# Kernel tuning notes

Hardware: AMD Instinct MI355X
Metric: run time of the kernel (lower is better)

Reference implementation:

```python
import jax, jax.numpy as jnp
import numpy as np

EPS = 1e-12  # F.normalize denominator clamp


def setup_inputs() -> dict:
    key = jax.random.key(0)
    k1, k2, k3, k4 = jax.random.split(key, 4)
    bs, d, nc, ncl, cs, ny = 8192, 768, 64, 500, 100, 1000
    train_embedding = jax.random.normal(k1, (bs, d), dtype=jnp.float32)
    clusters = jax.random.normal(k2, (ncl, cs, d), dtype=jnp.float32)
    # init_concept: uniform in [-0.5, 0.5]
    concept = jax.random.uniform(k3, (d, nc), dtype=jnp.float32, minval=-0.5, maxval=0.5)
    W_h = jax.random.normal(k4, (d, ny), dtype=jnp.float32) * 0.02
    b_h = jnp.zeros((ny,), dtype=jnp.float32)
    return {"train_embedding": train_embedding, "clusters": clusters,
            "concept": concept, "W_h": W_h, "b_h": b_h}


def reference(train_embedding, clusters, concept, W_h, b_h):
    # column-wise L2 normalize concept (F.normalize p=2 dim=0)
    concept_normalized = concept / jnp.maximum(
        jnp.linalg.norm(concept, axis=0, keepdims=True), EPS)
    # projection onto span(concept): C (C^T C)^-1 C^T
    gram = concept.T @ concept                      # [nc, nc]
    proj_matrix = concept @ jnp.linalg.inv(gram) @ concept.T  # [d, d]
    proj = proj_matrix @ train_embedding.T          # [d, bs]
    cluster_mean = jnp.mean(clusters, axis=1)       # [ncl, d]
    score_matrix = jnp.abs(cluster_mean @ concept_normalized)  # [ncl, nc]
    score_norm = score_matrix / jnp.maximum(
        jnp.linalg.norm(score_matrix, axis=0, keepdims=True), EPS)
    L_sparse_1 = jnp.sum(score_norm)
    # sum_{i != j} <score_norm[:,i], score_norm[:,j]> == sum(G) - trace(G)
    G = score_norm.T @ score_norm                   # [nc, nc]
    L_sparse_2 = jnp.sum(G) - jnp.trace(G)
    y_pred = proj.T @ W_h + b_h                     # h_x as linear head, [bs, ny]
    return (y_pred, L_sparse_1, L_sparse_2)
```

## Files before the change

kernel.cpp:

```cpp
#include <hip/hip_runtime.h>
#include <hip/hip_bf16.h>
#include <math.h>

#define BS   8192
#define DD   768
#define NC   64
#define NCL  500
#define CS   100
#define NY   1000
#define EPSN 1e-12f

typedef __attribute__((ext_vector_type(8))) short bf16x8;
typedef __attribute__((ext_vector_type(4))) float f32x4;

union B8 { unsigned u[4]; bf16x8 v; uint4 q; };

__device__ inline unsigned short f2bf(float x) {
    __hip_bfloat16 h = __float2bfloat16(x);
    return *reinterpret_cast<unsigned short*>(&h);
}
__device__ inline unsigned pk2(float a, float b) {
    return (unsigned)f2bf(a) | ((unsigned)f2bf(b) << 16);
}

#define FMA4(acc, s, v) { (acc).x = fmaf((s), (v).x, (acc).x); \
                          (acc).y = fmaf((s), (v).y, (acc).y); \
                          (acc).z = fmaf((s), (v).z, (acc).z); \
                          (acc).w = fmaf((s), (v).w, (acc).w); }

__global__ __launch_bounds__(256) void k_front(
    const float* __restrict__ clusters, const float* __restrict__ C,
    const float* __restrict__ W, const float* __restrict__ X,
    float* __restrict__ gramP, float* __restrict__ Up,
    float* __restrict__ SP, unsigned short* __restrict__ Tb) {
    __shared__ __align__(16) char smem_raw[25600];
    int b = blockIdx.x, tid = threadIdx.x;
    if (b < 200) {
        int rt = b / 25, sp = b % 25;
        uint4 (*CbL)[64] = (uint4(*)[64])smem_raw;
        int r0 = rt * 64;
        int w  = tid >> 6, l = tid & 63;
        int rowA = r0 + w*16 + (l & 15);
        int rcl  = rowA < NCL ? rowA : (NCL - 1);
        int kq   = l >> 4;
        const float* ab = clusters + (size_t)rcl * CS * DD + (size_t)sp * 4 * DD + kq * 8;
        f32x4 acc[4];
        #pragma unroll
        for (int ng = 0; ng < 4; ++ng) acc[ng] = (f32x4){0.f, 0.f, 0.f, 0.f};
        for (int kc = 0; kc < DD; kc += 64) {
            __syncthreads();
            #pragma unroll
            for (int u = 0; u < 2; ++u) {
                int g = (tid >> 6) + u*4;
                int n = tid & 63;
                const float* cp = C + (size_t)(kc + g*8) * 64 + n;
                uint4 gr;
                gr.x = pk2(cp[0],   cp[64]);
                gr.y = pk2(cp[128], cp[192]);
                gr.z = pk2(cp[256], cp[320]);
                gr.w = pk2(cp[384], cp[448]);
                CbL[g][n] = gr;
            }
            __syncthreads();
            #pragma unroll
            for (int ss = 0; ss < 4; ++ss) {
                #pragma unroll
                for (int ks2 = 0; ks2 < 2; ++ks2) {
                    const float* ap = ab + (size_t)ss * DD + kc + ks2*32;
                    float4 xa = *((const float4*)ap);
                    float4 xc = *((const float4*)(ap + 4));
                    B8 a;
                    a.u[0] = pk2(xa.x, xa.y); a.u[1] = pk2(xa.z, xa.w);
                    a.u[2] = pk2(xc.x, xc.y); a.u[3] = pk2(xc.z, xc.w);
                    B8 b0, b1, b2, b3;
                    b0.q = CbL[ks2*4 + kq][(l & 15)];
                    b1.q = CbL[ks2*4 + kq][(l & 15) + 16];
                    b2.q = CbL[ks2*4 + kq][(l & 15) + 32];
                    b3.q = CbL[ks2*4 + kq][(l & 15) + 48];
                    acc[0] = __builtin_amdgcn_mfma_f32_16x16x32_bf16(a.v, b0.v, acc[0], 0, 0, 0);
                    acc[1] = __builtin_amdgcn_mfma_f32_16x16x32_bf16(a.v, b1.v, acc[1], 0, 0, 0);
                    acc[2] = __builtin_amdgcn_mfma_f32_16x16x32_bf16(a.v, b2.v, acc[2], 0, 0, 0);
                    acc[3] = __builtin_amdgcn_mfma_f32_16x16x32_bf16(a.v, b3.v, acc[3], 0, 0, 0);
                }
            }
        }
        int rw = r0 + w*16 + kq * 4;
        float* SPs = SP + (size_t)sp * 32768;
        #pragma unroll
        for (int ng = 0; ng < 4; ++ng) {
            int n = ng*16 + (l & 15);
            #pragma unroll
            for (int r = 0; r < 4; ++r)
                SPs[(size_t)(rw + r) * 64 + n] = acc[ng][r];
        }
    } else if (b < 328) {
        uint4 (*CbL)[64] = (uint4(*)[64])smem_raw;
        int r0 = (b - 200) * 64;
        int w  = tid >> 6, l = tid & 63;
        int rowA = r0 + w*16 + (l & 15);
        int kq   = l >> 4;
        const float* xb = X + (size_t)rowA * DD + kq * 8;
        f32x4 acc[4];
        #pragma unroll
        for (int ng = 0; ng < 4; ++ng) acc[ng] = (f32x4){0.f, 0.f, 0.f, 0.f};
        for (int kc = 0; kc < DD; kc += 64) {
            __syncthreads();
            #pragma unroll
            for (int u = 0; u < 2; ++u) {
                int g = (tid >> 6) + u*4;
                int n = tid & 63;
                const float* cp = C + (size_t)(kc + g*8) * 64 + n;
                uint4 gr;
                gr.x = pk2(cp[0],   cp[64]);
                gr.y = pk2(cp[128], cp[192]);
                gr.z = pk2(cp[256], cp[320]);
                gr.w = pk2(cp[384], cp[448]);
                CbL[g][n] = gr;
            }
            __syncthreads();
            #pragma unroll
            for (int ks2 = 0; ks2 < 2; ++ks2) {
                float4 xa = *((const float4*)(xb + kc + ks2*32));
                float4 xc = *((const float4*)(xb + kc + ks2*32 + 4));
                B8 a;
                a.u[0] = pk2(xa.x, xa.y); a.u[1] = pk2(xa.z, xa.w);
                a.u[2] = pk2(xc.x, xc.y); a.u[3] = pk2(xc.z, xc.w);
                B8 b0, b1, b2, b3;
                b0.q = CbL[ks2*4 + kq][(l & 15)];
                b1.q = CbL[ks2*4 + kq][(l & 15) + 16];
                b2.q = CbL[ks2*4 + kq][(l & 15) + 32];
                b3.q = CbL[ks2*4 + kq][(l & 15) + 48];
                acc[0] = __builtin_amdgcn_mfma_f32_16x16x32_bf16(a.v, b0.v, acc[0], 0, 0, 0);
                acc[1] = __builtin_amdgcn_mfma_f32_16x16x32_bf16(a.v, b1.v, acc[1], 0, 0, 0);
                acc[2] = __builtin_amdgcn_mfma_f32_16x16x32_bf16(a.v, b2.v, acc[2], 0, 0, 0);
                acc[3] = __builtin_amdgcn_mfma_f32_16x16x32_bf16(a.v, b3.v, acc[3], 0, 0, 0);
            }
        }
        int rw = r0 + w*16 + kq * 4;
        #pragma unroll
        for (int ng = 0; ng < 4; ++ng) {
            int n = ng*16 + (l & 15);
            #pragma unroll
            for (int r = 0; r < 4; ++r)
                Tb[(size_t)(rw + r) * 64 + n] = f2bf(acc[ng][r]);
        }
    } else if (b < 584) {
        int q  = b - 328;
        int j  = q & 63, ks = q >> 6;
        int i   = tid & 63;
        int seg = tid >> 6;
        int k0  = ks * 192 + seg * 48;
        float p = 0.f;
        for (int k = k0; k < k0 + 48; ++k)
            p += C[k * NC + i] * C[k * NC + j];
        float (*red)[64] = (float(*)[64])smem_raw;
        red[seg][i] = p;
        __syncthreads();
        if (seg == 0)
            gramP[(size_t)ks * 4096 + i * NC + j] =
                red[0][i] + red[1][i] + red[2][i] + red[3][i];
    } else {
        int q  = b - 584;
        int nt = q >> 2, ks = q & 3;
        int n0 = nt * 128, kb = ks * 192;
        float (*Cu)[68]  = (float(*)[68])smem_raw;
        float (*Wu)[132] = (float(*)[132])(smem_raw + 8704);
        int tx = tid & 15, ty = tid >> 4;
        float4 a0[4], a1[4];
        #pragma unroll
        for (int i = 0; i < 4; ++i) { a0[i] = make_float4(0,0,0,0); a1[i] = make_float4(0,0,0,0); }
        for (int kc = kb; kc < kb + 192; kc += 32) {
            __syncthreads();
            {   int i4 = tid & 15, kk = tid >> 4;
                *((float4*)&Cu[kk][i4*4])    = *((const float4*)(C + (size_t)(kc+kk)*64 + i4*4));
                *((float4*)&Cu[kk+16][i4*4]) = *((const float4*)(C + (size_t)(kc+kk+16)*64 + i4*4));
            }
            {   int nf = tid & 31, kq2 = tid >> 5;
                #pragma unroll
                for (int u = 0; u < 4; ++u) {
                    int k = kq2 + u * 8;
                    int n = n0 + nf * 4;
                    float4 v = {0.f, 0.f, 0.f, 0.f};
                    if (n < NY) v = *((const float4*)(W + (size_t)(kc + k) * NY + n));
                    *((float4*)&Wu[k][nf*4]) = v;
                }
            }
            __syncthreads();
            #pragma unroll 8
            for (int k = 0; k < 32; ++k) {
                float4 ci = *((float4*)&Cu[k][ty*4]);
                float4 w0 = *((float4*)&Wu[k][tx*8]);
                float4 w1 = *((float4*)&Wu[k][tx*8+4]);
                FMA4(a0[0], ci.x, w0); FMA4(a1[0], ci.x, w1);
                FMA4(a0[1], ci.y, w0); FMA4(a1[1], ci.y, w1);
                FMA4(a0[2], ci.z, w0); FMA4(a1[2], ci.z, w1);
                FMA4(a0[3], ci.w, w0); FMA4(a1[3], ci.w, w1);
            }
        }
        float* Ups = Up + (size_t)ks * 64000;
        #pragma unroll
        for (int i = 0; i < 4; ++i) {
            int irow = ty * 4 + i;
            int n = n0 + tx * 8;
            if (n < NY)     *((float4*)(Ups + (size_t)irow * NY + n))     = a0[i];
            if (n + 4 < NY) *((float4*)(Ups + (size_t)irow * NY + n + 4)) = a1[i];
        }
    }
}

__global__ __launch_bounds__(256) void k_mid(
    const float* __restrict__ gramP, const float* __restrict__ SP,
    float* __restrict__ ginv, float* __restrict__ Sfin) {
    int blk = blockIdx.x, tid = threadIdx.x;
    if (blk == 0) {
        int c = tid & 63;
        int q = tid >> 6;
        float a[16], bb[16];
        #pragma unroll
        for (int i = 0; i < 16; ++i) {
            int r = q * 16 + i;
            size_t off = (size_t)r * 64 + c;
            a[i]  = gramP[off] + gramP[4096 + off] + gramP[8192 + off] + gramP[12288 + off];
            bb[i] = (r == c) ? 1.f : 0.f;
        }
        __shared__ float asr[2][64];
        __shared__ float bsr[2][64];
        for (int p = 0; p < 64; ++p) {
            int qp  = p >> 4;
            int lp  = p & 15;
            int par = p & 1;
            if (q == qp) {
                float ap = 0.f, bp = 0.f;
                #pragma unroll
                for (int i = 0; i < 16; ++i)
                    if (i == lp) { ap = a[i]; bp = bb[i]; }
                float App = __shfl(ap, p);
                float s   = 1.0f / App;
                asr[par][c] = ap * s;
                bsr[par][c] = bp * s;
            }
            __syncthreads();
            float as_ = asr[par][c];
            float bs_ = bsr[par][c];
            #pragma unroll
            for (int i = 0; i < 16; ++i) {
                float f = __shfl(a[i], p);
                bool isp = (q == qp) && (i == lp);
                a[i]  = isp ? as_ : fmaf(-f, as_, a[i]);
                bb[i] = isp ? bs_ : fmaf(-f, bs_, bb[i]);
            }
        }
        #pragma unroll
        for (int i = 0; i < 16; ++i)
            ginv[(q * 16 + i) * 64 + c] = bb[i];
    } else {
        int e = blk - 1;
        for (int t = tid; t < 1000; t += 256) {
            size_t off = (size_t)e * 4000 + (size_t)t * 4;
            float4 s = {0.f, 0.f, 0.f, 0.f};
            #pragma unroll
            for (int p = 0; p < 25; ++p) {
                float4 v = *((const float4*)(SP + (size_t)p * 32768 + off));
                s.x += v.x; s.y += v.y; s.z += v.z; s.w += v.w;
            }
            float4 o = {fabsf(s.x), fabsf(s.y), fabsf(s.z), fabsf(s.w)};
            *((float4*)(Sfin + off)) = o;
        }
    }
}

__global__ __launch_bounds__(256) void k_vc(
    const float* __restrict__ ginv, const float* __restrict__ Up,
    const float* __restrict__ Sfin, unsigned short* __restrict__ Vb,
    float* __restrict__ out2) {
    __shared__ __align__(16) char smem_raw[34816];
    int blk = blockIdx.x, tid = threadIdx.x;
    if (blk == 16) {
        __shared__ float colred[4][64];
        __shared__ float rn[64];
        __shared__ float trc[64];
        __shared__ float r1[4], r2[4];
        int c = tid & 63, seg = tid >> 6;
        float p = 0.f;
        for (int r = seg; r < NCL; r += 4) {
            float s = Sfin[r * 64 + c];
            p += s * s;
        }
        colred[seg][c] = p;
        __syncthreads();
        if (seg == 0) {
            float n2  = colred[0][c] + colred[1][c] + colred[2][c] + colred[3][c];
            float inv = 1.0f / fmaxf(sqrtf(n2), EPSN);
            rn[c]  = inv;
            trc[c] = n2 * inv * inv;
        }
        __syncthreads();
        float l1p = 0.f, l2p = 0.f;
        for (int r = tid; r < NCL; r += 256) {
            float rs = 0.f;
            #pragma unroll
            for (int cc = 0; cc < 64; ++cc)
                rs += Sfin[r * 64 + cc] * rn[cc];
            l1p += rs;
            l2p += rs * rs;
        }
        #pragma unroll
        for (int off = 32; off > 0; off >>= 1) {
            l1p += __shfl_down(l1p, off);
            l2p += __shfl_down(l2p, off);
        }
        int wave = tid >> 6, lane = tid & 63;
        if (lane == 0) { r1[wave] = l1p; r2[wave] = l2p; }
        __syncthreads();
        if (tid == 0) {
            float L1 = r1[0] + r1[1] + r1[2] + r1[3];
            float L2 = r2[0] + r2[1] + r2[2] + r2[3];
            float tr = 0.f;
            #pragma unroll
            for (int cc = 0; cc < 64; ++cc) tr += trc[cc];
            out2[0] = L1;
            out2[1] = L2 - tr;
        }
        return;
    }
    float (*Us)[68] = (float(*)[68])smem_raw;
    float (*Gs)[68] = (float(*)[68])(smem_raw + 64*68*4);
    int c0 = blk * 64;
    int tx = tid & 15, ty = tid >> 4;
    const float* Up0 = Up;
    const float* Up1 = Up + 64000;
    const float* Up2 = Up + 128000;
    const float* Up3 = Up + 192000;
    #pragma unroll
    for (int p = 0; p < 4; ++p) {
        int f = tid + p * 256;
        int j = f >> 4, n4 = f & 15;
        int n = c0 + n4 * 4;
        float4 v = {0.f, 0.f, 0.f, 0.f};
        if (n < NY) {
            float4 u0 = *((const float4*)(Up0 + (size_t)j * NY + n));
            float4 u1 = *((const float4*)(Up1 + (size_t)j * NY + n));
            float4 u2 = *((const float4*)(Up2 + (size_t)j * NY + n));
            float4 u3 = *((const float4*)(Up3 + (size_t)j * NY + n));
            v.x = u0.x + u1.x + u2.x + u3.x;
            v.y = u0.y + u1.y + u2.y + u3.y;
            v.z = u0.z + u1.z + u2.z + u3.z;
            v.w = u0.w + u1.w + u2.w + u3.w;
        }
        *((float4*)&Us[j][n4*4]) = v;
        *((float4*)&Gs[j][n4*4]) = *((const float4*)(ginv + (size_t)j * 64 + n4*4));
    }
    __syncthreads();
    float4 acc[4];
    #pragma unroll
    for (int i = 0; i < 4; ++i) acc[i] = make_float4(0.f,0.f,0.f,0.f);
    for (int j0 = 0; j0 < 64; j0 += 4) {
        #pragma unroll
        for (int jj = 0; jj < 4; ++jj) {
            float4 g = *((float4*)&Gs[j0+jj][ty*4]);
            float4 u = *((float4*)&Us[j0+jj][tx*4]);
            FMA4(acc[0], g.x, u);
            FMA4(acc[1], g.y, u);
            FMA4(acc[2], g.z, u);
            FMA4(acc[3], g.w, u);
        }
    }
    #pragma unroll
    for (int i = 0; i < 4; ++i) {
        int krow = ty * 4 + i;
        Vb[(size_t)(c0 + tx*4 + 0) * 64 + krow] = f2bf(acc[i].x);
        Vb[(size_t)(c0 + tx*4 + 1) * 64 + krow] = f2bf(acc[i].y);
        Vb[(size_t)(c0 + tx*4 + 2) * 64 + krow] = f2bf(acc[i].z);
        Vb[(size_t)(c0 + tx*4 + 3) * 64 + krow] = f2bf(acc[i].w);
    }
}

__global__ __launch_bounds__(256) void k_ypred(
    const uint4* __restrict__ Tb, const uint4* __restrict__ Vbq,
    const float* __restrict__ bh, float* __restrict__ Y) {
    int blk = blockIdx.x, tid = threadIdx.x;
    int rb = blk >> 3, cb = blk & 7;
    int r0g = rb * 128, c0g = cb * 128;
    int w = tid >> 6, l = tid & 63;
    int wr = (w >> 1) * 64, wc = (w & 1) * 64;
    int kq = l >> 4, ln = l & 15;
    f32x4 acc[4][4];
    #pragma unroll
    for (int rg = 0; rg < 4; ++rg)
        #pragma unroll
        for (int ng = 0; ng < 4; ++ng) acc[rg][ng] = (f32x4){0.f,0.f,0.f,0.f};
    #pragma unroll
    for (int ks = 0; ks < 2; ++ks) {
        B8 a[4], bb[4];
        #pragma unroll
        for (int rg = 0; rg < 4; ++rg) {
            int row = r0g + wr + rg*16 + ln;
            a[rg].q = Tb[(size_t)row * 8 + ks*4 + kq];
        }
        #pragma unroll
        for (int ng = 0; ng < 4; ++ng) {
            int n = c0g + wc + ng*16 + ln;
            bb[ng].q = Vbq[(size_t)n * 8 + ks*4 + kq];
        }
        #pragma unroll
        for (int rg = 0; rg < 4; ++rg)
            #pragma unroll
            for (int ng = 0; ng < 4; ++ng)
                acc[rg][ng] = __builtin_amdgcn_mfma_f32_16x16x32_bf16(
                    a[rg].v, bb[ng].v, acc[rg][ng], 0, 0, 0);
    }
    #pragma unroll
    for (int ng = 0; ng < 4; ++ng) {
        int n = c0g + wc + ng*16 + ln;
        if (n < NY) {
            float bias = bh[n];
            #pragma unroll
            for (int rg = 0; rg < 4; ++rg) {
                int row = r0g + wr + rg*16 + kq*4;
                #pragma unroll
                for (int r = 0; r < 4; ++r)
                    Y[(size_t)(row + r) * NY + n] = acc[rg][ng][r] + bias;
            }
        }
    }
}

extern "C" void kernel_launch(void* const* d_in, const int* in_sizes, int n_in,
                              void* d_out, int out_size, void* d_ws, size_t ws_size,
                              hipStream_t stream) {
    const float* X        = (const float*)d_in[0];
    const float* clusters = (const float*)d_in[1];
    const float* C        = (const float*)d_in[2];
    const float* W        = (const float*)d_in[3];
    const float* bh       = (const float*)d_in[4];
    float* out = (float*)d_out;
    float* ws  = (float*)d_ws;

    float* gramP = ws;
    float* ginv  = gramP + 16384;
    float* Up    = ginv  + 4096;
    float* SP    = Up    + 256000;
    float* Sfin  = SP    + 819200;
    float* TbF   = Sfin  + 32768;
    float* VbF   = TbF   + 262144;

    unsigned short* Tb  = (unsigned short*)TbF;
    unsigned short* Vb  = (unsigned short*)VbF;

    k_front <<<dim3(616), dim3(256), 0, stream>>>(clusters, C, W, X, gramP, Up, SP, Tb);
    k_mid   <<<dim3(9),   dim3(256), 0, stream>>>(gramP, SP, ginv, Sfin);
    k_vc    <<<dim3(17),  dim3(256), 0, stream>>>(ginv, Up, Sfin, Vb, out + (size_t)BS * NY);
    k_ypred <<<dim3(512), dim3(256), 0, stream>>>((const uint4*)Tb, (const uint4*)Vb, bh, out);
}
```

Measured before the change: 146.6 us.

## Split front-kernel work finer and shrink ypred tiles for more parallelism

Cluster-score blocks now each cover 2 samples instead of 4 (50 partial slabs instead of 25). The X·C projection is split into two K-halves that write fp32 partials, and k_ypred sums them and converts to bf16 when loading A. k_ypred tiles shrink to 64 rows, so twice as many blocks launch. The intent is to fill more CUs in the front and final kernels, at the cost of extra partial-sum traffic (larger SP and fp32 Tp) and a longer reduction in k_mid.

```diff
diff --git a/kernel.cpp b/kernel.cpp
--- a/kernel.cpp
+++ b/kernel.cpp
@@ -32,18 +32,18 @@
     const float* __restrict__ clusters, const float* __restrict__ C,
     const float* __restrict__ W, const float* __restrict__ X,
     float* __restrict__ gramP, float* __restrict__ Up,
-    float* __restrict__ SP, unsigned short* __restrict__ Tb) {
+    float* __restrict__ SP, float* __restrict__ Tp) {
     __shared__ __align__(16) char smem_raw[25600];
     int b = blockIdx.x, tid = threadIdx.x;
-    if (b < 200) {
-        int rt = b / 25, sp = b % 25;
+    if (b < 400) {
+        int rt = b / 50, sp = b % 50;
         uint4 (*CbL)[64] = (uint4(*)[64])smem_raw;
         int r0 = rt * 64;
         int w  = tid >> 6, l = tid & 63;
         int rowA = r0 + w*16 + (l & 15);
         int rcl  = rowA < NCL ? rowA : (NCL - 1);
         int kq   = l >> 4;
-        const float* ab = clusters + (size_t)rcl * CS * DD + (size_t)sp * 4 * DD + kq * 8;
+        const float* ab = clusters + (size_t)rcl * CS * DD + (size_t)sp * 2 * DD + kq * 8;
         f32x4 acc[4];
         #pragma unroll
         for (int ng = 0; ng < 4; ++ng) acc[ng] = (f32x4){0.f, 0.f, 0.f, 0.f};
@@ -63,7 +63,7 @@
             }
             __syncthreads();
             #pragma unroll
-            for (int ss = 0; ss < 4; ++ss) {
+            for (int ss = 0; ss < 2; ++ss) {
                 #pragma unroll
                 for (int ks2 = 0; ks2 < 2; ++ks2) {
                     const float* ap = ab + (size_t)ss * DD + kc + ks2*32;
@@ -93,9 +93,11 @@
             for (int r = 0; r < 4; ++r)
                 SPs[(size_t)(rw + r) * 64 + n] = acc[ng][r];
         }
-    } else if (b < 328) {
+    } else if (b < 656) {
+        int q = b - 400;
+        int tile = q >> 1, ksg = q & 1;
         uint4 (*CbL)[64] = (uint4(*)[64])smem_raw;
-        int r0 = (b - 200) * 64;
+        int r0 = tile * 64;
         int w  = tid >> 6, l = tid & 63;
         int rowA = r0 + w*16 + (l & 15);
         int kq   = l >> 4;
@@ -103,7 +105,8 @@
         f32x4 acc[4];
         #pragma unroll
         for (int ng = 0; ng < 4; ++ng) acc[ng] = (f32x4){0.f, 0.f, 0.f, 0.f};
-        for (int kc = 0; kc < DD; kc += 64) {
+        int base = ksg * 384;
+        for (int kc = base; kc < base + 384; kc += 64) {
             __syncthreads();
             #pragma unroll
             for (int u = 0; u < 2; ++u) {
@@ -137,15 +140,16 @@
             }
         }
         int rw = r0 + w*16 + kq * 4;
+        float* Tps = Tp + (size_t)ksg * BS * 64;
         #pragma unroll
         for (int ng = 0; ng < 4; ++ng) {
             int n = ng*16 + (l & 15);
             #pragma unroll
             for (int r = 0; r < 4; ++r)
-                Tb[(size_t)(rw + r) * 64 + n] = f2bf(acc[ng][r]);
-        }
-    } else if (b < 584) {
-        int q  = b - 328;
+                Tps[(size_t)(rw + r) * 64 + n] = acc[ng][r];
+        }
+    } else if (b < 912) {
+        int q  = b - 656;
         int j  = q & 63, ks = q >> 6;
         int i   = tid & 63;
         int seg = tid >> 6;
@@ -160,7 +164,7 @@
             gramP[(size_t)ks * 4096 + i * NC + j] =
                 red[0][i] + red[1][i] + red[2][i] + red[3][i];
     } else {
-        int q  = b - 584;
+        int q  = b - 912;
         int nt = q >> 2, ks = q & 3;
         int n0 = nt * 128, kb = ks * 192;
         float (*Cu)[68]  = (float(*)[68])smem_raw;
@@ -255,15 +259,18 @@
             ginv[(q * 16 + i) * 64 + c] = bb[i];
     } else {
         int e = blk - 1;
-        for (int t = tid; t < 1000; t += 256) {
-            size_t off = (size_t)e * 4000 + (size_t)t * 4;
-            float4 s = {0.f, 0.f, 0.f, 0.f};
-            #pragma unroll
-            for (int p = 0; p < 25; ++p) {
-                float4 v = *((const float4*)(SP + (size_t)p * 32768 + off));
-                s.x += v.x; s.y += v.y; s.z += v.z; s.w += v.w;
-            }
-            float4 o = {fabsf(s.x), fabsf(s.y), fabsf(s.z), fabsf(s.w)};
+        for (int t = tid; t < 500; t += 256) {
+            size_t off = (size_t)e * 2000 + (size_t)t * 4;
+            float4 s0 = {0.f,0.f,0.f,0.f}, s1 = {0.f,0.f,0.f,0.f};
+            #pragma unroll
+            for (int p = 0; p < 50; p += 2) {
+                float4 v0 = *((const float4*)(SP + (size_t)p * 32768 + off));
+                float4 v1 = *((const float4*)(SP + (size_t)(p+1) * 32768 + off));
+                s0.x += v0.x; s0.y += v0.y; s0.z += v0.z; s0.w += v0.w;
+                s1.x += v1.x; s1.y += v1.y; s1.z += v1.z; s1.w += v1.w;
+            }
+            float4 o = {fabsf(s0.x + s1.x), fabsf(s0.y + s1.y),
+                        fabsf(s0.z + s1.z), fabsf(s0.w + s1.w)};
             *((float4*)(Sfin + off)) = o;
         }
     }
@@ -376,26 +383,37 @@
 }
 
 __global__ __launch_bounds__(256) void k_ypred(
-    const uint4* __restrict__ Tb, const uint4* __restrict__ Vbq,
+    const float* __restrict__ Tp, const uint4* __restrict__ Vbq,
     const float* __restrict__ bh, float* __restrict__ Y) {
     int blk = blockIdx.x, tid = threadIdx.x;
     int rb = blk >> 3, cb = blk & 7;
-    int r0g = rb * 128, c0g = cb * 128;
+    int r0g = rb * 64, c0g = cb * 128;
     int w = tid >> 6, l = tid & 63;
-    int wr = (w >> 1) * 64, wc = (w & 1) * 64;
+    int wrow = (w >> 1) * 32, wc = (w & 1) * 64;
     int kq = l >> 4, ln = l & 15;
-    f32x4 acc[4][4];
-    #pragma unroll
-    for (int rg = 0; rg < 4; ++rg)
+    const float* Tp0 = Tp;
+    const float* Tp1 = Tp + (size_t)BS * 64;
+    f32x4 acc[2][4];
+    #pragma unroll
+    for (int rg = 0; rg < 2; ++rg)
         #pragma unroll
         for (int ng = 0; ng < 4; ++ng) acc[rg][ng] = (f32x4){0.f,0.f,0.f,0.f};
     #pragma unroll
     for (int ks = 0; ks < 2; ++ks) {
-        B8 a[4], bb[4];
-        #pragma unroll
-        for (int rg = 0; rg < 4; ++rg) {
-            int row = r0g + wr + rg*16 + ln;
-            a[rg].q = Tb[(size_t)row * 8 + ks*4 + kq];
+        B8 a[2], bb[4];
+        #pragma unroll
+        for (int rg = 0; rg < 2; ++rg) {
+            int row = r0g + wrow + rg*16 + ln;
+            const float* t0 = Tp0 + (size_t)row * 64 + ks*32 + kq*8;
+            const float* t1 = Tp1 + (size_t)row * 64 + ks*32 + kq*8;
+            float4 p0 = *((const float4*)t0);
+            float4 p1 = *((const float4*)(t0 + 4));
+            float4 q0 = *((const float4*)t1);
+            float4 q1 = *((const float4*)(t1 + 4));
+            a[rg].u[0] = pk2(p0.x + q0.x, p0.y + q0.y);
+            a[rg].u[1] = pk2(p0.z + q0.z, p0.w + q0.w);
+            a[rg].u[2] = pk2(p1.x + q1.x, p1.y + q1.y);
+            a[rg].u[3] = pk2(p1.z + q1.z, p1.w + q1.w);
         }
         #pragma unroll
         for (int ng = 0; ng < 4; ++ng) {
@@ -403,7 +421,7 @@
             bb[ng].q = Vbq[(size_t)n * 8 + ks*4 + kq];
         }
         #pragma unroll
-        for (int rg = 0; rg < 4; ++rg)
+        for (int rg = 0; rg < 2; ++rg)
             #pragma unroll
             for (int ng = 0; ng < 4; ++ng)
                 acc[rg][ng] = __builtin_amdgcn_mfma_f32_16x16x32_bf16(
@@ -415,8 +433,8 @@
         if (n < NY) {
             float bias = bh[n];
             #pragma unroll
-            for (int rg = 0; rg < 4; ++rg) {
-                int row = r0g + wr + rg*16 + kq*4;
+            for (int rg = 0; rg < 2; ++rg) {
+                int row = r0g + wrow + rg*16 + kq*4;
                 #pragma unroll
                 for (int r = 0; r < 4; ++r)
                     Y[(size_t)(row + r) * NY + n] = acc[rg][ng][r] + bias;
@@ -440,15 +458,14 @@
     float* ginv  = gramP + 16384;
     float* Up    = ginv  + 4096;
     float* SP    = Up    + 256000;
-    float* Sfin  = SP    + 819200;
-    float* TbF   = Sfin  + 32768;
-    float* VbF   = TbF   + 262144;
-
-    unsigned short* Tb  = (unsigned short*)TbF;
-    unsigned short* Vb  = (unsigned short*)VbF;
-
-    k_front <<<dim3(616), dim3(256), 0, stream>>>(clusters, C, W, X, gramP, Up, SP, Tb);
-    k_mid   <<<dim3(9),   dim3(256), 0, stream>>>(gramP, SP, ginv, Sfin);
-    k_vc    <<<dim3(17),  dim3(256), 0, stream>>>(ginv, Up, Sfin, Vb, out + (size_t)BS * NY);
-    k_ypred <<<dim3(512), dim3(256), 0, stream>>>((const uint4*)Tb, (const uint4*)Vb, bh, out);
-}
+    float* Sfin  = SP    + 1638400;
+    float* Tp    = Sfin  + 32768;
+    float* VbF   = Tp    + 1048576;
+
+    unsigned short* Vb = (unsigned short*)VbF;
+
+    k_front <<<dim3(944),  dim3(256), 0, stream>>>(clusters, C, W, X, gramP, Up, SP, Tp);
+    k_mid   <<<dim3(17),   dim3(256), 0, stream>>>(gramP, SP, ginv, Sfin);
+    k_vc    <<<dim3(17),   dim3(256), 0, stream>>>(ginv, Up, Sfin, Vb, out + (size_t)BS * NY);
+    k_ypred <<<dim3(1024), dim3(256), 0, stream>>>(Tp, (const uint4*)Vb, bh, out);
+}
```

Result: slower. 152.3 us (+3.9%).

## Split cluster-score GEMM over K halves and software-pipeline A loads in front kernel

Applied to the files above, without the earlier changes.

The cluster-score branch now splits the K dimension into two halves, doubling its block count to 400 and the partial-sum buffer to 50 slices. Each block stages its whole half of the concept matrix in LDS once, instead of re-staging it every 64 columns with barriers. Global A loads are double-buffered in registers so loads overlap MFMA work, and the X-projection branch gets the same treatment. The reduction kernel uses more blocks and two accumulators to sum the 50 partials. The cost is larger LDS (48KB, which may reduce occupancy) and twice the partial-sum traffic.

```diff
diff --git a/kernel.cpp b/kernel.cpp
--- a/kernel.cpp
+++ b/kernel.cpp
@@ -28,124 +28,154 @@
                           (acc).z = fmaf((s), (v).z, (acc).z); \
                           (acc).w = fmaf((s), (v).w, (acc).w); }
 
+#define MFMA_(a, b, c) __builtin_amdgcn_mfma_f32_16x16x32_bf16((a).v, (b).v, (c), 0, 0, 0)
+
 __global__ __launch_bounds__(256) void k_front(
     const float* __restrict__ clusters, const float* __restrict__ C,
     const float* __restrict__ W, const float* __restrict__ X,
     float* __restrict__ gramP, float* __restrict__ Up,
     float* __restrict__ SP, unsigned short* __restrict__ Tb) {
-    __shared__ __align__(16) char smem_raw[25600];
+    __shared__ __align__(16) char smem_raw[49152];
     int b = blockIdx.x, tid = threadIdx.x;
-    if (b < 200) {
-        int rt = b / 25, sp = b % 25;
+    if (b < 400) {
+        int rt = b / 50, q2 = b % 50, sp = q2 >> 1, ks = q2 & 1;
+        int kb = ks * 384;
         uint4 (*CbL)[64] = (uint4(*)[64])smem_raw;
         int r0 = rt * 64;
         int w  = tid >> 6, l = tid & 63;
-        int rowA = r0 + w*16 + (l & 15);
+        int l15 = l & 15;
+        int rowA = r0 + w*16 + l15;
         int rcl  = rowA < NCL ? rowA : (NCL - 1);
         int kq   = l >> 4;
-        const float* ab = clusters + (size_t)rcl * CS * DD + (size_t)sp * 4 * DD + kq * 8;
+        const float* ab = clusters + (size_t)rcl * CS * DD + (size_t)sp * 4 * DD
+                        + kb + kq * 8;
+        #pragma unroll
+        for (int u = 0; u < 12; ++u) {
+            int gi = (tid >> 6) + u * 4;
+            int n  = tid & 63;
+            const float* cp = C + (size_t)(kb + gi*8) * 64 + n;
+            uint4 gr;
+            gr.x = pk2(cp[0],   cp[64]);
+            gr.y = pk2(cp[128], cp[192]);
+            gr.z = pk2(cp[256], cp[320]);
+            gr.w = pk2(cp[384], cp[448]);
+            CbL[gi][n] = gr;
+        }
+        __syncthreads();
         f32x4 acc[4];
         #pragma unroll
         for (int ng = 0; ng < 4; ++ng) acc[ng] = (f32x4){0.f, 0.f, 0.f, 0.f};
-        for (int kc = 0; kc < DD; kc += 64) {
-            __syncthreads();
-            #pragma unroll
-            for (int u = 0; u < 2; ++u) {
-                int g = (tid >> 6) + u*4;
-                int n = tid & 63;
-                const float* cp = C + (size_t)(kc + g*8) * 64 + n;
+        float4 A0[8], A1[8];
+        #define LOADA(dst, c) { \
+            dst[0] = *(const float4*)(ab + (c)*32); \
+            dst[1] = *(const float4*)(ab + (c)*32 + 4); \
+            dst[2] = *(const float4*)(ab + DD + (c)*32); \
+            dst[3] = *(const float4*)(ab + DD + (c)*32 + 4); \
+            dst[4] = *(const float4*)(ab + 2*DD + (c)*32); \
+            dst[5] = *(const float4*)(ab + 2*DD + (c)*32 + 4); \
+            dst[6] = *(const float4*)(ab + 3*DD + (c)*32); \
+            dst[7] = *(const float4*)(ab + 3*DD + (c)*32 + 4); }
+        #define COMPS(src, c) { \
+            B8 b0, b1, b2, b3; \
+            b0.q = CbL[(c)*4 + kq][l15];      b1.q = CbL[(c)*4 + kq][l15 + 16]; \
+            b2.q = CbL[(c)*4 + kq][l15 + 32]; b3.q = CbL[(c)*4 + kq][l15 + 48]; \
+            _Pragma("unroll") \
+            for (int ss = 0; ss < 4; ++ss) { \
+                B8 a; \
+                a.u[0] = pk2(src[ss*2].x,   src[ss*2].y); \
+                a.u[1] = pk2(src[ss*2].z,   src[ss*2].w); \
+                a.u[2] = pk2(src[ss*2+1].x, src[ss*2+1].y); \
+                a.u[3] = pk2(src[ss*2+1].z, src[ss*2+1].w); \
+                acc[0] = MFMA_(a, b0, acc[0]); acc[1] = MFMA_(a, b1, acc[1]); \
+                acc[2] = MFMA_(a, b2, acc[2]); acc[3] = MFMA_(a, b3, acc[3]); } }
+        LOADA(A0, 0);
+        #pragma unroll
+        for (int c = 0; c < 12; c += 2) {
+            LOADA(A1, c + 1);
+            COMPS(A0, c);
+            if (c + 2 < 12) LOADA(A0, c + 2);
+            COMPS(A1, c + 1);
+        }
+        #undef LOADA
+        #undef COMPS
+        int rw = r0 + w*16 + kq * 4;
+        float* SPs = SP + (size_t)(sp * 2 + ks) * 32768;
+        #pragma unroll
+        for (int ng = 0; ng < 4; ++ng) {
+            int n = ng*16 + l15;
+            #pragma unroll
+            for (int r = 0; r < 4; ++r)
+                SPs[(size_t)(rw + r) * 64 + n] = acc[ng][r];
+        }
+    } else if (b < 528) {
+        uint4 (*CbL)[64] = (uint4(*)[64])smem_raw;
+        int r0 = (b - 400) * 64;
+        int w  = tid >> 6, l = tid & 63;
+        int l15 = l & 15;
+        int rowA = r0 + w*16 + l15;
+        int kq   = l >> 4;
+        f32x4 acc[4];
+        #pragma unroll
+        for (int ng = 0; ng < 4; ++ng) acc[ng] = (f32x4){0.f, 0.f, 0.f, 0.f};
+        #pragma unroll
+        for (int half = 0; half < 2; ++half) {
+            int kb = half * 384;
+            if (half) __syncthreads();
+            #pragma unroll
+            for (int u = 0; u < 12; ++u) {
+                int gi = (tid >> 6) + u * 4;
+                int n  = tid & 63;
+                const float* cp = C + (size_t)(kb + gi*8) * 64 + n;
                 uint4 gr;
                 gr.x = pk2(cp[0],   cp[64]);
                 gr.y = pk2(cp[128], cp[192]);
                 gr.z = pk2(cp[256], cp[320]);
                 gr.w = pk2(cp[384], cp[448]);
-                CbL[g][n] = gr;
+                CbL[gi][n] = gr;
             }
             __syncthreads();
-            #pragma unroll
-            for (int ss = 0; ss < 4; ++ss) {
-                #pragma unroll
-                for (int ks2 = 0; ks2 < 2; ++ks2) {
-                    const float* ap = ab + (size_t)ss * DD + kc + ks2*32;
-                    float4 xa = *((const float4*)ap);
-                    float4 xc = *((const float4*)(ap + 4));
-                    B8 a;
-                    a.u[0] = pk2(xa.x, xa.y); a.u[1] = pk2(xa.z, xa.w);
-                    a.u[2] = pk2(xc.x, xc.y); a.u[3] = pk2(xc.z, xc.w);
-                    B8 b0, b1, b2, b3;
-                    b0.q = CbL[ks2*4 + kq][(l & 15)];
-                    b1.q = CbL[ks2*4 + kq][(l & 15) + 16];
-                    b2.q = CbL[ks2*4 + kq][(l & 15) + 32];
-                    b3.q = CbL[ks2*4 + kq][(l & 15) + 48];
-                    acc[0] = __builtin_amdgcn_mfma_f32_16x16x32_bf16(a.v, b0.v, acc[0], 0, 0, 0);
-                    acc[1] = __builtin_amdgcn_mfma_f32_16x16x32_bf16(a.v, b1.v, acc[1], 0, 0, 0);
-                    acc[2] = __builtin_amdgcn_mfma_f32_16x16x32_bf16(a.v, b2.v, acc[2], 0, 0, 0);
-                    acc[3] = __builtin_amdgcn_mfma_f32_16x16x32_bf16(a.v, b3.v, acc[3], 0, 0, 0);
-                }
-            }
+            const float* xh = X + (size_t)rowA * DD + kb + kq * 8;
+            float4 A0[4], A1[4];
+            #define LOADX(dst, c) { \
+                dst[0] = *(const float4*)(xh + (c)*32); \
+                dst[1] = *(const float4*)(xh + (c)*32 + 4); \
+                dst[2] = *(const float4*)(xh + (c)*32 + 32); \
+                dst[3] = *(const float4*)(xh + (c)*32 + 36); }
+            #define COMPX(src, c) { \
+                _Pragma("unroll") \
+                for (int cc = 0; cc < 2; ++cc) { \
+                    B8 b0, b1, b2, b3, a; \
+                    b0.q = CbL[((c)+cc)*4 + kq][l15]; \
+                    b1.q = CbL[((c)+cc)*4 + kq][l15 + 16]; \
+                    b2.q = CbL[((c)+cc)*4 + kq][l15 + 32]; \
+                    b3.q = CbL[((c)+cc)*4 + kq][l15 + 48]; \
+                    a.u[0] = pk2(src[cc*2].x,   src[cc*2].y); \
+                    a.u[1] = pk2(src[cc*2].z,   src[cc*2].w); \
+                    a.u[2] = pk2(src[cc*2+1].x, src[cc*2+1].y); \
+                    a.u[3] = pk2(src[cc*2+1].z, src[cc*2+1].w); \
+                    acc[0] = MFMA_(a, b0, acc[0]); acc[1] = MFMA_(a, b1, acc[1]); \
+                    acc[2] = MFMA_(a, b2, acc[2]); acc[3] = MFMA_(a, b3, acc[3]); } }
+            LOADX(A0, 0);
+            #pragma unroll
+            for (int s = 0; s < 6; s += 2) {
+                LOADX(A1, (s + 1) * 2);
+                COMPX(A0, s * 2);
+                if (s + 2 < 6) LOADX(A0, (s + 2) * 2);
+                COMPX(A1, (s + 1) * 2);
+            }
+            #undef LOADX
+            #undef COMPX
         }
         int rw = r0 + w*16 + kq * 4;
-        float* SPs = SP + (size_t)sp * 32768;
         #pragma unroll
         for (int ng = 0; ng < 4; ++ng) {
-            int n = ng*16 + (l & 15);
-            #pragma unroll
-            for (int r = 0; r < 4; ++r)
-                SPs[(size_t)(rw + r) * 64 + n] = acc[ng][r];
-        }
-    } else if (b < 328) {
-        uint4 (*CbL)[64] = (uint4(*)[64])smem_raw;
-        int r0 = (b - 200) * 64;
-        int w  = tid >> 6, l = tid & 63;
-        int rowA = r0 + w*16 + (l & 15);
-        int kq   = l >> 4;
-        const float* xb = X + (size_t)rowA * DD + kq * 8;
-        f32x4 acc[4];
-        #pragma unroll
-        for (int ng = 0; ng < 4; ++ng) acc[ng] = (f32x4){0.f, 0.f, 0.f, 0.f};
-        for (int kc = 0; kc < DD; kc += 64) {
-            __syncthreads();
-            #pragma unroll
-            for (int u = 0; u < 2; ++u) {
-                int g = (tid >> 6) + u*4;
-                int n = tid & 63;
-                const float* cp = C + (size_t)(kc + g*8) * 64 + n;
-                uint4 gr;
-                gr.x = pk2(cp[0],   cp[64]);
-                gr.y = pk2(cp[128], cp[192]);
-                gr.z = pk2(cp[256], cp[320]);
-                gr.w = pk2(cp[384], cp[448]);
-                CbL[g][n] = gr;
-            }
-            __syncthreads();
-            #pragma unroll
-            for (int ks2 = 0; ks2 < 2; ++ks2) {
-                float4 xa = *((const float4*)(xb + kc + ks2*32));
-                float4 xc = *((const float4*)(xb + kc + ks2*32 + 4));
-                B8 a;
-                a.u[0] = pk2(xa.x, xa.y); a.u[1] = pk2(xa.z, xa.w);
-                a.u[2] = pk2(xc.x, xc.y); a.u[3] = pk2(xc.z, xc.w);
-                B8 b0, b1, b2, b3;
-                b0.q = CbL[ks2*4 + kq][(l & 15)];
-                b1.q = CbL[ks2*4 + kq][(l & 15) + 16];
-                b2.q = CbL[ks2*4 + kq][(l & 15) + 32];
-                b3.q = CbL[ks2*4 + kq][(l & 15) + 48];
-                acc[0] = __builtin_amdgcn_mfma_f32_16x16x32_bf16(a.v, b0.v, acc[0], 0, 0, 0);
-                acc[1] = __builtin_amdgcn_mfma_f32_16x16x32_bf16(a.v, b1.v, acc[1], 0, 0, 0);
-                acc[2] = __builtin_amdgcn_mfma_f32_16x16x32_bf16(a.v, b2.v, acc[2], 0, 0, 0);
-                acc[3] = __builtin_amdgcn_mfma_f32_16x16x32_bf16(a.v, b3.v, acc[3], 0, 0, 0);
-            }
-        }
-        int rw = r0 + w*16 + kq * 4;
-        #pragma unroll
-        for (int ng = 0; ng < 4; ++ng) {
-            int n = ng*16 + (l & 15);
+            int n = ng*16 + l15;
             #pragma unroll
             for (int r = 0; r < 4; ++r)
                 Tb[(size_t)(rw + r) * 64 + n] = f2bf(acc[ng][r]);
         }
-    } else if (b < 584) {
-        int q  = b - 328;
+    } else if (b < 784) {
+        int q  = b - 528;
         int j  = q & 63, ks = q >> 6;
         int i   = tid & 63;
         int seg = tid >> 6;
@@ -160,7 +190,7 @@
             gramP[(size_t)ks * 4096 + i * NC + j] =
                 red[0][i] + red[1][i] + red[2][i] + red[3][i];
     } else {
-        int q  = b - 584;
+        int q  = b - 784;
         int nt = q >> 2, ks = q & 3;
         int n0 = nt * 128, kb = ks * 192;
         float (*Cu)[68]  = (float(*)[68])smem_raw;
@@ -255,15 +285,18 @@
             ginv[(q * 16 + i) * 64 + c] = bb[i];
     } else {
         int e = blk - 1;
-        for (int t = tid; t < 1000; t += 256) {
-            size_t off = (size_t)e * 4000 + (size_t)t * 4;
-            float4 s = {0.f, 0.f, 0.f, 0.f};
-            #pragma unroll
-            for (int p = 0; p < 25; ++p) {
-                float4 v = *((const float4*)(SP + (size_t)p * 32768 + off));
-                s.x += v.x; s.y += v.y; s.z += v.z; s.w += v.w;
-            }
-            float4 o = {fabsf(s.x), fabsf(s.y), fabsf(s.z), fabsf(s.w)};
+        for (int t = tid; t < 500; t += 256) {
+            size_t off = (size_t)e * 2000 + (size_t)t * 4;
+            float4 s0 = {0.f,0.f,0.f,0.f}, s1 = {0.f,0.f,0.f,0.f};
+            #pragma unroll
+            for (int p = 0; p < 50; p += 2) {
+                float4 v0 = *((const float4*)(SP + (size_t)p * 32768 + off));
+                float4 v1 = *((const float4*)(SP + (size_t)(p+1) * 32768 + off));
+                s0.x += v0.x; s0.y += v0.y; s0.z += v0.z; s0.w += v0.w;
+                s1.x += v1.x; s1.y += v1.y; s1.z += v1.z; s1.w += v1.w;
+            }
+            float4 o = {fabsf(s0.x + s1.x), fabsf(s0.y + s1.y),
+                        fabsf(s0.z + s1.z), fabsf(s0.w + s1.w)};
             *((float4*)(Sfin + off)) = o;
         }
     }
@@ -376,7 +409,7 @@
 }
 
 __global__ __launch_bounds__(256) void k_ypred(
-    const uint4* __restrict__ Tb, const uint4* __restrict__ Vbq,
+    const uint4* __restrict__ Tbq, const uint4* __restrict__ Vbq,
     const float* __restrict__ bh, float* __restrict__ Y) {
     int blk = blockIdx.x, tid = threadIdx.x;
     int rb = blk >> 3, cb = blk & 7;
@@ -395,7 +428,7 @@
         #pragma unroll
         for (int rg = 0; rg < 4; ++rg) {
             int row = r0g + wr + rg*16 + ln;
-            a[rg].q = Tb[(size_t)row * 8 + ks*4 + kq];
+            a[rg].q = Tbq[(size_t)row * 8 + ks*4 + kq];
         }
         #pragma unroll
         for (int ng = 0; ng < 4; ++ng) {
@@ -440,15 +473,15 @@
     float* ginv  = gramP + 16384;
     float* Up    = ginv  + 4096;
     float* SP    = Up    + 256000;
-    float* Sfin  = SP    + 819200;
+    float* Sfin  = SP    + 1638400;
     float* TbF   = Sfin  + 32768;
     float* VbF   = TbF   + 262144;
 
-    unsigned short* Tb  = (unsigned short*)TbF;
-    unsigned short* Vb  = (unsigned short*)VbF;
-
-    k_front <<<dim3(616), dim3(256), 0, stream>>>(clusters, C, W, X, gramP, Up, SP, Tb);
-    k_mid   <<<dim3(9),   dim3(256), 0, stream>>>(gramP, SP, ginv, Sfin);
+    unsigned short* Tb = (unsigned short*)TbF;
+    unsigned short* Vb = (unsigned short*)VbF;
+
+    k_front <<<dim3(816), dim3(256), 0, stream>>>(clusters, C, W, X, gramP, Up, SP, Tb);
+    k_mid   <<<dim3(17),  dim3(256), 0, stream>>>(gramP, SP, ginv, Sfin);
     k_vc    <<<dim3(17),  dim3(256), 0, stream>>>(ginv, Up, Sfin, Vb, out + (size_t)BS * NY);
     k_ypred <<<dim3(512), dim3(256), 0, stream>>>((const uint4*)Tb, (const uint4*)Vb, bh, out);
 }
```

New measurement: 155.9 us. 1.06x slower.

## Fuse V computation into y_pred kernel, building V tile in shared memory

Applied to the files above, without the earlier changes.

Merges the k_vc kernel into k_ypred. Each output block now reduces the Up partials and multiplies by ginv for its own 128-column slice, then stores the bf16 V tile in LDS instead of global memory. This removes one kernel launch and the global write and read of Vb. In exchange each of the 64 row blocks per column slice recomputes the same 64x128 V tile, and LDS use grows to about 68KB per block, which may reduce occupancy.

```diff
diff --git a/kernel.cpp b/kernel.cpp
--- a/kernel.cpp
+++ b/kernel.cpp
@@ -269,13 +269,14 @@
     }
 }
 
-__global__ __launch_bounds__(256) void k_vc(
-    const float* __restrict__ ginv, const float* __restrict__ Up,
-    const float* __restrict__ Sfin, unsigned short* __restrict__ Vb,
+__global__ __launch_bounds__(256) void k_ypred(
+    const uint4* __restrict__ Tbq, const float* __restrict__ ginv,
+    const float* __restrict__ Up, const float* __restrict__ Sfin,
+    const float* __restrict__ bh, float* __restrict__ Y,
     float* __restrict__ out2) {
-    __shared__ __align__(16) char smem_raw[34816];
+    __shared__ __align__(16) char smem_raw[69632];
     int blk = blockIdx.x, tid = threadIdx.x;
-    if (blk == 16) {
+    if (blk == 512) {
         __shared__ float colred[4][64];
         __shared__ float rn[64];
         __shared__ float trc[64];
@@ -323,64 +324,76 @@
         }
         return;
     }
-    float (*Us)[68] = (float(*)[68])smem_raw;
-    float (*Gs)[68] = (float(*)[68])(smem_raw + 64*68*4);
-    int c0 = blk * 64;
-    int tx = tid & 15, ty = tid >> 4;
-    const float* Up0 = Up;
-    const float* Up1 = Up + 64000;
-    const float* Up2 = Up + 128000;
-    const float* Up3 = Up + 192000;
-    #pragma unroll
-    for (int p = 0; p < 4; ++p) {
-        int f = tid + p * 256;
-        int j = f >> 4, n4 = f & 15;
-        int n = c0 + n4 * 4;
-        float4 v = {0.f, 0.f, 0.f, 0.f};
-        if (n < NY) {
-            float4 u0 = *((const float4*)(Up0 + (size_t)j * NY + n));
-            float4 u1 = *((const float4*)(Up1 + (size_t)j * NY + n));
-            float4 u2 = *((const float4*)(Up2 + (size_t)j * NY + n));
-            float4 u3 = *((const float4*)(Up3 + (size_t)j * NY + n));
-            v.x = u0.x + u1.x + u2.x + u3.x;
-            v.y = u0.y + u1.y + u2.y + u3.y;
-            v.z = u0.z + u1.z + u2.z + u3.z;
-            v.w = u0.w + u1.w + u2.w + u3.w;
-        }
-        *((float4*)&Us[j][n4*4]) = v;
-        *((float4*)&Gs[j][n4*4]) = *((const float4*)(ginv + (size_t)j * 64 + n4*4));
-    }
-    __syncthreads();
-    float4 acc[4];
-    #pragma unroll
-    for (int i = 0; i < 4; ++i) acc[i] = make_float4(0.f,0.f,0.f,0.f);
-    for (int j0 = 0; j0 < 64; j0 += 4) {
-        #pragma unroll
-        for (int jj = 0; jj < 4; ++jj) {
-            float4 g = *((float4*)&Gs[j0+jj][ty*4]);
-            float4 u = *((float4*)&Us[j0+jj][tx*4]);
-            FMA4(acc[0], g.x, u);
-            FMA4(acc[1], g.y, u);
-            FMA4(acc[2], g.z, u);
-            FMA4(acc[3], g.w, u);
-        }
-    }
-    #pragma unroll
-    for (int i = 0; i < 4; ++i) {
-        int krow = ty * 4 + i;
-        Vb[(size_t)(c0 + tx*4 + 0) * 64 + krow] = f2bf(acc[i].x);
-        Vb[(size_t)(c0 + tx*4 + 1) * 64 + krow] = f2bf(acc[i].y);
-        Vb[(size_t)(c0 + tx*4 + 2) * 64 + krow] = f2bf(acc[i].z);
-        Vb[(size_t)(c0 + tx*4 + 3) * 64 + krow] = f2bf(acc[i].w);
-    }
-}
-
-__global__ __launch_bounds__(256) void k_ypred(
-    const uint4* __restrict__ Tb, const uint4* __restrict__ Vbq,
-    const float* __restrict__ bh, float* __restrict__ Y) {
-    int blk = blockIdx.x, tid = threadIdx.x;
+    float (*Gs)[68]  = (float(*)[68])smem_raw;
+    float (*Us)[132] = (float(*)[132])(smem_raw + 17408);
+    unsigned short* VbL = (unsigned short*)(smem_raw + 17408 + 33792);
     int rb = blk >> 3, cb = blk & 7;
     int r0g = rb * 128, c0g = cb * 128;
+    {
+        #pragma unroll
+        for (int p = 0; p < 4; ++p) {
+            int f = tid + p * 256;
+            int j = f >> 4, n4 = f & 15;
+            *((float4*)&Gs[j][n4*4]) = *((const float4*)(ginv + (size_t)j * 64 + n4*4));
+        }
+    }
+    {
+        const float* Up0 = Up;
+        const float* Up1 = Up + 64000;
+        const float* Up2 = Up + 128000;
+        const float* Up3 = Up + 192000;
+        #pragma unroll
+        for (int p = 0; p < 8; ++p) {
+            int f = tid + p * 256;
+            int j = f >> 5, n8 = f & 31;
+            int n = c0g + n8 * 4;
+            float4 v = {0.f, 0.f, 0.f, 0.f};
+            if (n < NY) {
+                float4 u0 = *((const float4*)(Up0 + (size_t)j * NY + n));
+                float4 u1 = *((const float4*)(Up1 + (size_t)j * NY + n));
+                float4 u2 = *((const float4*)(Up2 + (size_t)j * NY + n));
+                float4 u3 = *((const float4*)(Up3 + (size_t)j * NY + n));
+                v.x = u0.x + u1.x + u2.x + u3.x;
+                v.y = u0.y + u1.y + u2.y + u3.y;
+                v.z = u0.z + u1.z + u2.z + u3.z;
+                v.w = u0.w + u1.w + u2.w + u3.w;
+            }
+            *((float4*)&Us[j][n8*4]) = v;
+        }
+    }
+    __syncthreads();
+    int tx = tid & 31, ty = tid >> 5;
+    float4 vr[2][4];
+    #pragma unroll
+    for (int rh = 0; rh < 2; ++rh)
+        #pragma unroll
+        for (int i = 0; i < 4; ++i) vr[rh][i] = make_float4(0.f, 0.f, 0.f, 0.f);
+    #pragma unroll
+    for (int rh = 0; rh < 2; ++rh) {
+        int k0 = rh * 32 + ty * 4;
+        #pragma unroll 4
+        for (int j = 0; j < 64; ++j) {
+            float4 g = *((float4*)&Gs[j][k0]);
+            float4 u = *((float4*)&Us[j][tx*4]);
+            FMA4(vr[rh][0], g.x, u);
+            FMA4(vr[rh][1], g.y, u);
+            FMA4(vr[rh][2], g.z, u);
+            FMA4(vr[rh][3], g.w, u);
+        }
+    }
+    #pragma unroll
+    for (int rh = 0; rh < 2; ++rh) {
+        #pragma unroll
+        for (int i = 0; i < 4; ++i) {
+            int k = rh * 32 + ty * 4 + i;
+            int base = (k >> 3) * 8 + (k & 7);
+            VbL[(tx*4 + 0) * 72 + base] = f2bf(vr[rh][i].x);
+            VbL[(tx*4 + 1) * 72 + base] = f2bf(vr[rh][i].y);
+            VbL[(tx*4 + 2) * 72 + base] = f2bf(vr[rh][i].z);
+            VbL[(tx*4 + 3) * 72 + base] = f2bf(vr[rh][i].w);
+        }
+    }
+    __syncthreads();
     int w = tid >> 6, l = tid & 63;
     int wr = (w >> 1) * 64, wc = (w & 1) * 64;
     int kq = l >> 4, ln = l & 15;
@@ -395,12 +408,12 @@
         #pragma unroll
         for (int rg = 0; rg < 4; ++rg) {
             int row = r0g + wr + rg*16 + ln;
-            a[rg].q = Tb[(size_t)row * 8 + ks*4 + kq];
+            a[rg].q = Tbq[(size_t)row * 8 + ks*4 + kq];
         }
         #pragma unroll
         for (int ng = 0; ng < 4; ++ng) {
-            int n = c0g + wc + ng*16 + ln;
-            bb[ng].q = Vbq[(size_t)n * 8 + ks*4 + kq];
+            int nl = wc + ng*16 + ln;
+            bb[ng].q = *((const uint4*)(VbL + nl*72 + (ks*4 + kq)*8));
         }
         #pragma unroll
         for (int rg = 0; rg < 4; ++rg)
@@ -442,13 +455,11 @@
     float* SP    = Up    + 256000;
     float* Sfin  = SP    + 819200;
     float* TbF   = Sfin  + 32768;
-    float* VbF   = TbF   + 262144;
-
-    unsigned short* Tb  = (unsigned short*)TbF;
-    unsigned short* Vb  = (unsigned short*)VbF;
+
+    unsigned short* Tb = (unsigned short*)TbF;
 
     k_front <<<dim3(616), dim3(256), 0, stream>>>(clusters, C, W, X, gramP, Up, SP, Tb);
     k_mid   <<<dim3(9),   dim3(256), 0, stream>>>(gramP, SP, ginv, Sfin);
-    k_vc    <<<dim3(17),  dim3(256), 0, stream>>>(ginv, Up, Sfin, Vb, out + (size_t)BS * NY);
-    k_ypred <<<dim3(512), dim3(256), 0, stream>>>((const uint4*)Tb, (const uint4*)Vb, bh, out);
-}
+    k_ypred <<<dim3(513), dim3(256), 0, stream>>>((const uint4*)Tb, ginv, Up, Sfin,
+                                                  bh, out, out + (size_t)BS * NY);
+}
```

New measurement: 149.2 us. Within noise of the previous version (+1.8%).
